# Kernel optimization log

Measured on AMD Instinct MI355X. Metric: run time of the kernel, lower is better.

The kernel has to match this reference:

```python
import jax, jax.numpy as jnp
import numpy as np
from jax import lax

STRIDE = 2
PADDING = 2
KSIZE = 5


def _maxpool3d(y, k):
    # valid max pool with kernel=stride=k over the 3 spatial dims of NCDHW
    return lax.reduce_window(
        y, -jnp.inf, lax.max,
        window_dimensions=(1, 1, k, k, k),
        window_strides=(1, 1, k, k, k),
        padding='VALID')


def setup_inputs() -> dict:
    key = jax.random.key(0)
    k1, k2, k3 = jax.random.split(key, 3)
    x = jax.random.normal(k1, (16, 32, 16, 32, 32), dtype=jnp.float32)
    # torch ConvTranspose3d weight layout: (in_ch, out_ch, kD, kH, kW)
    weight = jax.random.normal(k2, (32, 64, KSIZE, KSIZE, KSIZE), dtype=jnp.float32) * 0.05
    bias = jax.random.normal(k3, (64,), dtype=jnp.float32) * 0.05
    return {"x": x, "weight": weight, "bias": bias}


def reference(x, weight, bias):
    # Fused ConvTranspose3d + sum over output channels.
    # sum_c convT(x, W)[:, c] == convT(x, W.sum(out_ch)) + bias.sum(), so we
    # pre-reduce the weight over the out-channel axis (axis=1) -- same math,
    # and it never materializes the (N, out_ch, D', H', W') intermediate,
    # exactly like the fused CUDA kernel.
    w_sum = weight.sum(axis=1)  # (in_ch, kD, kH, kW)
    # transposed conv == conv with lhs_dilation=stride, pad k-1-p, flipped kernel
    wk = w_sum[None, :, ::-1, ::-1, ::-1]  # (1, in_ch, kD, kH, kW), OIDHW
    pad = KSIZE - 1 - PADDING
    y = lax.conv_general_dilated(
        x, wk,
        window_strides=(1, 1, 1),
        padding=[(pad, pad)] * 3,
        lhs_dilation=(STRIDE, STRIDE, STRIDE),
        dimension_numbers=('NCDHW', 'OIDHW', 'NCDHW'))  # (N,1,31,63,63)
    y = y + bias.sum()
    # MaxPool3d(kernel=2) then MaxPool3d(kernel=3) on the single-channel map
    y = _maxpool3d(y, 2)  # (N,1,15,31,31)
    y = _maxpool3d(y, 3)  # (N,1,5,10,10)
    return y
```

## Files before the change

### kernel.cpp

```cpp
#include <hip/hip_runtime.h>


typedef short v8s __attribute__((ext_vector_type(8)));
typedef float v4f __attribute__((ext_vector_type(4)));
typedef unsigned short ushort_t;

#define CHSTR 16384
#define NSTRIDE (32*CHSTR)
#define Y_N 108000
#define Y_TOT (16*Y_N)
#define XSTR 24

#define PLANE_US 36992u
#define ROW_US 1088u
#define XTN16 591872u
#define BT_BYTE_OFF 18939904u
#define WSF_BYTE_OFF 18967552u
#define NEED_MFMA (18967552u + 4097u*4u)

static __device__ __forceinline__ ushort_t f2bf(float f) {
  unsigned u = __builtin_bit_cast(unsigned, f);
  unsigned r = (u + 0x7FFFu + ((u >> 16) & 1u)) >> 16;
  return (ushort_t)r;
}

__global__ __launch_bounds__(576) void transpose_x(const float* __restrict__ x,
                                                   const float* __restrict__ wt,
                                                   const float* __restrict__ bias,
                                                   ushort_t* __restrict__ xT,
                                                   ushort_t* __restrict__ Btab,
                                                   float* __restrict__ wsf) {
  __shared__ __align__(16) float lb[32 * 264];
  int b = blockIdx.x, t = threadIdx.x;

  if (b >= 256) {
    if (t < 256) {
      int abc = b - 256;
      int a = abc / 9, bb = (abc / 3) % 3, c = abc % 3;
      int half = t & 3;
      int l = t >> 2;
      int tt = l & 15, g = l >> 4;
      float v0 = 0.f, v1 = 0.f;
      if (tt < 8) {
        int td = tt & 1, th = (tt >> 1) & 1, tw = tt >> 2;
        int kd = td + 2 * a, kh = th + 2 * bb, kw = tw + 2 * c;
        if (kd < 5 && kh < 5 && kw < 5) {
          int off = kd * 25 + kh * 5 + kw;
          const float* wp0 = wt + (size_t)(8 * g + 2 * half) * 64 * 125 + off;
          const float* wp1 = wp0 + 64 * 125;
          float s0 = 0.f, s1 = 0.f;
#pragma unroll
          for (int oc = 0; oc < 64; ++oc) { s0 += wp0[oc * 125]; s1 += wp1[oc * 125]; }
          v0 = s0; v1 = s1;
        }
      }
      ((unsigned*)Btab)[(abc * 64 + l) * 4 + half] =
          (unsigned)f2bf(v0) | ((unsigned)f2bf(v1) << 16);
      if (abc == 0 && t == 0) {
        float bs = 0.f;
        for (int o = 0; o < 64; ++o) bs += bias[o];
        wsf[4096] = bs;
      }
    }
    return;
  }

  int tn = 2 * (b & 7) + ((b >> 3) & 1);
  int q  = b >> 4;
  ushort_t* plane = xT + (size_t)(tn * 16 + q) * PLANE_US;
  const float* xb = x + (size_t)tn * NSTRIDE + q * 1024;

  for (int cc = 0; cc < 4; ++cc) {
    for (int j = 0; j < 4; ++j) {
      int s2 = t + 576 * j;
      if (s2 < 2048) {
        int wq = s2 & 7, h8 = (s2 >> 3) & 7, ic = s2 >> 6;
        int h = 8 * cc - 1 + h8;
        if (h >= 0) {
          float4 v = *(const float4*)&xb[(size_t)ic * CHSTR + h * 32 + wq * 4];
          float* L = lb + ic * 264 + h8 * 33 + wq * 4;
          L[0] = v.x; L[1] = v.y; L[2] = v.z; L[3] = v.w;
        }
      }
    }
    __syncthreads();
    for (int j = 0; j < 2; ++j) {
      int s = t + 576 * j;
      if (s < 1088) {
        int icq = s & 3, qq = s >> 2;
        int wslot = qq % 34, r8 = qq / 34;
        int row = 8 * cc + r8;
        ushort_t o[8];
#pragma unroll
        for (int jj = 0; jj < 8; ++jj) o[jj] = 0;
        if (wslot >= 1 && wslot <= 32 && row > 0) {
          int w2 = wslot - 1;
#pragma unroll
          for (int jj = 0; jj < 8; ++jj)
            o[jj] = f2bf(lb[(8 * icq + jj) * 264 + r8 * 33 + w2]);
        }
        uint4 pk;
        pk.x = (unsigned)o[0] | ((unsigned)o[1] << 16);
        pk.y = (unsigned)o[2] | ((unsigned)o[3] << 16);
        pk.z = (unsigned)o[4] | ((unsigned)o[5] << 16);
        pk.w = (unsigned)o[6] | ((unsigned)o[7] << 16);
        *(uint4*)&plane[(size_t)row * ROW_US + wslot * 32 + icq * 8] = pk;
      }
    }
    __syncthreads();
  }
}

__global__ __launch_bounds__(576, 7) void conv_mfma6(const ushort_t* __restrict__ xT,
                                                     const ushort_t* __restrict__ Btab,
                                                     const float* __restrict__ wsf,
                                                     float* __restrict__ out) {
  __shared__ __align__(16) char smem[35328];
  ushort_t* As0 = (ushort_t*)smem;
  ushort_t* As1 = (ushort_t*)(smem + 17408);
  float* ytile  = (float*)smem;
  float* red    = (float*)(smem + 34816);

  int blk = blockIdx.x;
  int xcd = blk & 7;
  int j = blk >> 3;
  int n = 2 * xcd + (j >= 25 ? 1 : 0);
  int cell = (j >= 25) ? j - 25 : j;
  int OD = cell / 5, OH2 = cell % 5;

  int t = threadIdx.x;
  int wv = t >> 6, l = t & 63;
  int mdl = wv / 3, mhp = wv % 3;
  int tt = l & 15, g = l >> 4;

  const ushort_t* xn = xT + (size_t)n * XTN16;
  int rowoff = 6 * OH2 * (int)ROW_US;

  if (OD == 0) {
    for (int jj = 0; jj < 2; ++jj) {
      int s = t + 576 * jj;
      if (s < 1088) *(uint4*)&As0[s * 8] = make_uint4(0, 0, 0, 0);
    }
  } else {
    const ushort_t* slab = xn + (size_t)(3 * OD - 1) * PLANE_US + rowoff;
    uint4 v0 = *(const uint4*)(slab + (size_t)t * 8);
    uint4 v1;
    if (t < 512) v1 = *(const uint4*)(slab + (size_t)(t + 576) * 8);
    *(uint4*)&As0[t * 8] = v0;
    if (t < 512) *(uint4*)&As0[(t + 576) * 8] = v1;
  }
  __syncthreads();

  v4f acc[2][2];
#pragma unroll
  for (int m2 = 0; m2 < 2; ++m2)
#pragma unroll
    for (int wh = 0; wh < 2; ++wh) acc[m2][wh] = (v4f){0.f, 0.f, 0.f, 0.f};

  int lane_base = (2 * mhp) * ROW_US + tt * 32 + g * 8;

  for (int p = 0; p < 5; ++p) {
    uint4 v0, v1;
    if (p < 4) {
      const ushort_t* slab = xn + (size_t)(3 * OD + p) * PLANE_US + rowoff;
      v0 = *(const uint4*)(slab + (size_t)t * 8);
      if (t < 512) v1 = *(const uint4*)(slab + (size_t)(t + 576) * 8);
    }

    int a = mdl + 2 - p;
    if (0 <= a && a <= 2) {
      const ushort_t* Ab = (p & 1) ? As1 : As0;
      const ushort_t* Bg = Btab + ((size_t)(a * 9) * 64 + l) * 8;
      __builtin_amdgcn_s_setprio(1);
#pragma unroll
      for (int c = 0; c < 3; ++c) {
        v8s bv0 = *(const v8s*)(Bg + (0 * 3 + c) * 512);
        v8s bv1 = *(const v8s*)(Bg + (1 * 3 + c) * 512);
        v8s bv2 = *(const v8s*)(Bg + (2 * 3 + c) * 512);
#pragma unroll
        for (int wh = 0; wh < 2; ++wh) {
          const ushort_t* ap = Ab + lane_base + (2 - c + 16 * wh) * 32;
          v8s a0 = *(const v8s*)(ap);
          v8s a1 = *(const v8s*)(ap + 1 * ROW_US);
          v8s a2 = *(const v8s*)(ap + 2 * ROW_US);
          v8s a3 = *(const v8s*)(ap + 3 * ROW_US);
          acc[0][wh] = __builtin_amdgcn_mfma_f32_16x16x32_bf16(a0, bv2, acc[0][wh], 0, 0, 0);
          acc[0][wh] = __builtin_amdgcn_mfma_f32_16x16x32_bf16(a1, bv1, acc[0][wh], 0, 0, 0);
          acc[0][wh] = __builtin_amdgcn_mfma_f32_16x16x32_bf16(a2, bv0, acc[0][wh], 0, 0, 0);
          acc[1][wh] = __builtin_amdgcn_mfma_f32_16x16x32_bf16(a1, bv2, acc[1][wh], 0, 0, 0);
          acc[1][wh] = __builtin_amdgcn_mfma_f32_16x16x32_bf16(a2, bv1, acc[1][wh], 0, 0, 0);
          acc[1][wh] = __builtin_amdgcn_mfma_f32_16x16x32_bf16(a3, bv0, acc[1][wh], 0, 0, 0);
        }
      }
      __builtin_amdgcn_s_setprio(0);
    }

    if (p < 4) {
      ushort_t* dst = (p & 1) ? As0 : As1;
      *(uint4*)&dst[t * 8] = v0;
      if (t < 512) *(uint4*)&dst[(t + 576) * 8] = v1;
      __syncthreads();
    }
  }

  __syncthreads();
  if (tt < 8) {
    int td = tt & 1, th = (tt >> 1) & 1, tw = tt >> 2;
    int odl = 2 * mdl + td;
#pragma unroll
    for (int m2 = 0; m2 < 2; ++m2) {
      int ohl = 2 * (2 * mhp + m2) + th;
      float* yrow = &ytile[(odl * 12 + ohl) * 64];
#pragma unroll
      for (int wh = 0; wh < 2; ++wh)
#pragma unroll
        for (int i = 0; i < 4; ++i)
          yrow[2 * (16 * wh + 4 * g + i) + tw] = acc[m2][wh][i];
    }
  }
  __syncthreads();

  if (t < 120) {
    int OW = t % 10, p_oh = (t / 10) & 1, odl = t / 20;
    float m = -3.4e38f;
    for (int oh = 0; oh < 6; ++oh)
#pragma unroll
      for (int jj = 0; jj < 6; ++jj)
        m = fmaxf(m, ytile[(odl * 12 + 6 * p_oh + oh) * 64 + 6 * OW + jj]);
    red[t] = m;
  }
  __syncthreads();
  if (t < 20) {
    int OW = t % 10, p_oh = t / 10;
    float m = red[p_oh * 10 + OW];
#pragma unroll
    for (int odl = 1; odl < 6; ++odl) m = fmaxf(m, red[odl * 20 + p_oh * 10 + OW]);
    out[((n * 5 + OD) * 10 + (2 * OH2 + p_oh)) * 10 + OW] = m + wsf[4096];
  }
}

__global__ __launch_bounds__(128) void prep2(const float* __restrict__ w,
                                             const float* __restrict__ bias,
                                             float* __restrict__ ws, int woff) {
  int i = blockIdx.x, t = threadIdx.x;
  if (t < 125) {
    const float* wp = w + (size_t)i * 64 * 125 + t;
    float v = 0.f;
#pragma unroll
    for (int o = 0; o < 64; ++o) v += wp[o * 125];
    ws[woff + i * 128 + t] = v;
  }
  if (i == 0 && t == 126) {
    float b = 0.f;
    for (int o = 0; o < 64; ++o) b += bias[o];
    ws[woff + 4096] = b;
  }
}

__global__ __launch_bounds__(256, 4) void conv_stage1(const float* __restrict__ x,
                                                      const float* __restrict__ ws,
                                                      float* part, int woff) {
  __shared__ __align__(16) float xs[170 * XSTR];
  int blk = blockIdx.x;
  int s0 = blk % 320;
  int wq = s0 & 1, hq = (s0 >> 1) & 1, dc = (s0 >> 2) % 5, n = s0 / 20;
  int t = threadIdx.x;
  int mw = t % 15, lmh = t / 15;
  int id_base = 3 * dc - 1, ih_base = 15 * hq - 1;
  int iwb = wq ? 12 : -4;
  int cb = mw + (wq ? 2 : 3);
  const float* xn = x + (size_t)n * NSTRIDE;
  const float* wsw = ws + woff;
  float acc[3][2][2][2] = {{{{0.f}}}};
  for (int phs = 0; phs < 16; ++phs) {
    for (int s = t; s < 1700; s += 256) {
      int c2 = s % 10, row = s / 10;
      int bh = row % 17, q = row / 17;
      int ad = q % 5, lic = q / 5;
      int id = id_base + ad, ih = ih_base + bh, iw = iwb + 2 * c2;
      float2 v = make_float2(0.f, 0.f);
      if ((id | ih | iw) >= 0)
        v = *(const float2*)&xn[(size_t)(phs * 2 + lic) * CHSTR + (id * 32 + ih) * 32 + iw];
      *(float2*)&xs[row * XSTR + 2 * c2] = v;
    }
    __syncthreads();
    if (t < 225) {
#pragma unroll
      for (int lic = 0; lic < 2; ++lic) {
        const float* wc = wsw + (size_t)(phs * 2 + lic) * 128;
        const float* xc = &xs[(lic * 85 + lmh) * XSTR + cb];
        float xv[5][3][3];
#pragma unroll
        for (int a = 0; a < 5; ++a)
#pragma unroll
          for (int b = 0; b < 3; ++b) {
            const float* xr = xc + (a * 17 + b) * XSTR;
            xv[a][b][0] = xr[0]; xv[a][b][1] = xr[1]; xv[a][b][2] = xr[2];
          }
#pragma unroll
        for (int kd = 0; kd < 5; ++kd) {
          constexpr int DT[5] = {0, 1, 0, 1, 0};
          constexpr int AOFF[5] = {2, 2, 1, 1, 0};
          const int dt = DT[kd], aoff = AOFF[kd];
          float wvv[25];
#pragma unroll
          for (int jj = 0; jj < 25; ++jj) wvv[jj] = wc[kd * 25 + jj];
#pragma unroll
          for (int kh = 0; kh < 5; ++kh) {
            constexpr int HT[5] = {0, 1, 0, 1, 0};
            constexpr int BOFF[5] = {2, 2, 1, 1, 0};
            const int ht = HT[kh], boff = BOFF[kh];
#pragma unroll
            for (int m = 0; m < 3; ++m) {
              const float x0 = xv[m + aoff][boff][0];
              const float x1 = xv[m + aoff][boff][1];
              const float x2 = xv[m + aoff][boff][2];
              acc[m][dt][ht][0] += x0 * wvv[kh * 5 + 4];
              acc[m][dt][ht][0] += x1 * wvv[kh * 5 + 2];
              acc[m][dt][ht][0] += x2 * wvv[kh * 5 + 0];
              acc[m][dt][ht][1] += x1 * wvv[kh * 5 + 3];
              acc[m][dt][ht][1] += x2 * wvv[kh * 5 + 1];
            }
          }
        }
      }
    }
    __syncthreads();
  }
  if (t < 225) {
    float* pb = part + (size_t)n * Y_N;
#pragma unroll
    for (int m = 0; m < 3; ++m)
#pragma unroll
      for (int dt = 0; dt < 2; ++dt)
#pragma unroll
        for (int ht = 0; ht < 2; ++ht) {
          int od_g = 6 * dc + 2 * m + dt;
          int oh_g = 30 * hq + 2 * lmh + ht;
          int ow_g = 30 * wq + 2 * mw;
          *(float2*)&pb[(od_g * 60 + oh_g) * 60 + ow_g] =
              make_float2(acc[m][dt][ht][0], acc[m][dt][ht][1]);
        }
  }
}

__global__ __launch_bounds__(256) void pool_stage2(const float* __restrict__ part,
                                                   const float* __restrict__ ws,
                                                   float* __restrict__ out, int woff) {
  __shared__ __align__(16) float buf[2160];
  __shared__ float red[240];
  int blk = blockIdx.x;
  int hc = blk % 10, dc = (blk / 10) % 5, n = blk / 50;
  int t = threadIdx.x;
  const float* pb = part + (size_t)n * Y_N;
  for (int s = t; s < 540; s += 256) {
    int row = s / 15, c4 = s % 15;
    int od = row / 6, oh = row % 6;
    size_t idx = (size_t)((6 * dc + od) * 60 + (6 * hc + oh)) * 60 + 4 * c4;
    *(float4*)&buf[row * 60 + 4 * c4] = *(const float4*)&pb[idx];
  }
  __syncthreads();
  if (t < 240) {
    int wc = t / 24, sub = t % 24;
    float m = -3.4e38f;
#pragma unroll
    for (int k = 0; k < 9; ++k) {
      int e = sub + 24 * k;
      int od = e / 36, r = e % 36;
      int oh = r / 6, ow0 = r % 6;
      m = fmaxf(m, buf[(od * 6 + oh) * 60 + 6 * wc + ow0]);
    }
    red[t] = m;
  }
  __syncthreads();
  if (t < 10) {
    float mm = -3.4e38f;
#pragma unroll
    for (int s2 = 0; s2 < 24; ++s2) mm = fmaxf(mm, red[t * 24 + s2]);
    out[((n * 5 + dc) * 10 + hc) * 10 + t] = mm + ws[woff + 4096];
  }
}

extern "C" void kernel_launch(void* const* d_in, const int* in_sizes, int n_in,
                              void* d_out, int out_size, void* d_ws, size_t ws_size,
                              hipStream_t stream) {
  const float* x    = (const float*)d_in[0];
  const float* w    = (const float*)d_in[1];
  const float* bias = (const float*)d_in[2];
  float* outp = (float*)d_out;

  if (ws_size >= (size_t)NEED_MFMA) {
    ushort_t* xT = (ushort_t*)d_ws;
    ushort_t* Bt = (ushort_t*)((char*)d_ws + BT_BYTE_OFF);
    float* wsf   = (float*)((char*)d_ws + WSF_BYTE_OFF);
    transpose_x<<<256 + 27, 576, 0, stream>>>(x, w, bias, xT, Bt, wsf);
    conv_mfma6<<<400, 576, 0, stream>>>(xT, Bt, wsf, outp);
    return;
  }

  float* ws = (float*)d_ws;
  const size_t need1 = ((size_t)1 * Y_TOT + 4097) * 4;
  if (ws_size >= need1) {
    int woff = Y_TOT;
    prep2<<<32, 128, 0, stream>>>(w, bias, ws, woff);
    conv_stage1<<<320, 256, 0, stream>>>(x, ws, ws, woff);
    pool_stage2<<<800, 256, 0, stream>>>(ws, ws, outp, woff);
  }
}
```

Baseline: 32.09 us.

## Split conv blocks along width into halves to double grid size

The MFMA conv kernel now gives each block half of the output width, so the grid doubles from 400 to 800 blocks. The shared slab per block shrinks to a compacted row layout, and each wave keeps two accumulators instead of four. The goal is more blocks and less LDS per block for better occupancy and load balance across CUs. In exchange, neighbouring halves reload overlapping input halo columns and B-table loads, and the weight fetches are amortized over less work.

Measured after the change: 34.81 us. 8.5% more time.

```diff
diff --git a/kernel.cpp b/kernel.cpp
--- a/kernel.cpp
+++ b/kernel.cpp
@@ -17,6 +17,8 @@
 #define BT_BYTE_OFF 18939904u
 #define WSF_BYTE_OFF 18967552u
 #define NEED_MFMA (18967552u + 4097u*4u)
+
+#define SLAB_ROW 576
 
 static __device__ __forceinline__ ushort_t f2bf(float f) {
   unsigned u = __builtin_bit_cast(unsigned, f);
@@ -111,22 +113,24 @@
   }
 }
 
-__global__ __launch_bounds__(576, 7) void conv_mfma6(const ushort_t* __restrict__ xT,
+__global__ __launch_bounds__(576, 7) void conv_mfma8(const ushort_t* __restrict__ xT,
                                                      const ushort_t* __restrict__ Btab,
                                                      const float* __restrict__ wsf,
                                                      float* __restrict__ out) {
-  __shared__ __align__(16) char smem[35328];
+  __shared__ __align__(16) char smem[18672];
   ushort_t* As0 = (ushort_t*)smem;
-  ushort_t* As1 = (ushort_t*)(smem + 17408);
+  ushort_t* As1 = (ushort_t*)(smem + 9216);
   float* ytile  = (float*)smem;
-  float* red    = (float*)(smem + 34816);
+  float* red    = (float*)(smem + 18432);
 
   int blk = blockIdx.x;
   int xcd = blk & 7;
   int j = blk >> 3;
-  int n = 2 * xcd + (j >= 25 ? 1 : 0);
-  int cell = (j >= 25) ? j - 25 : j;
-  int OD = cell / 5, OH2 = cell % 5;
+  int n = 2 * xcd + (j >= 50 ? 1 : 0);
+  int c50 = (j >= 50) ? j - 50 : j;
+  int OD = c50 / 10;
+  int r10 = c50 % 10;
+  int OH2 = r10 >> 1, h = r10 & 1;
 
   int t = threadIdx.x;
   int wv = t >> 6, l = t & 63;
@@ -134,38 +138,29 @@
   int tt = l & 15, g = l >> 4;
 
   const ushort_t* xn = xT + (size_t)n * XTN16;
-  int rowoff = 6 * OH2 * (int)ROW_US;
+  const ushort_t* slabb = xn + (size_t)(6 * OH2) * ROW_US + 15 * h * 32;
+  int r8 = t / 72, inner = t % 72;
+  int colrel = inner >> 2, icq = inner & 3;
+  size_t soff = (size_t)r8 * ROW_US + colrel * 32 + icq * 8;
+  int doff = r8 * SLAB_ROW + colrel * 32 + icq * 8;
 
   if (OD == 0) {
-    for (int jj = 0; jj < 2; ++jj) {
-      int s = t + 576 * jj;
-      if (s < 1088) *(uint4*)&As0[s * 8] = make_uint4(0, 0, 0, 0);
-    }
+    *(uint4*)&As0[t * 16 / 2] = make_uint4(0, 0, 0, 0);
   } else {
-    const ushort_t* slab = xn + (size_t)(3 * OD - 1) * PLANE_US + rowoff;
-    uint4 v0 = *(const uint4*)(slab + (size_t)t * 8);
-    uint4 v1;
-    if (t < 512) v1 = *(const uint4*)(slab + (size_t)(t + 576) * 8);
-    *(uint4*)&As0[t * 8] = v0;
-    if (t < 512) *(uint4*)&As0[(t + 576) * 8] = v1;
-  }
-  __syncthreads();
-
-  v4f acc[2][2];
-#pragma unroll
-  for (int m2 = 0; m2 < 2; ++m2)
-#pragma unroll
-    for (int wh = 0; wh < 2; ++wh) acc[m2][wh] = (v4f){0.f, 0.f, 0.f, 0.f};
-
-  int lane_base = (2 * mhp) * ROW_US + tt * 32 + g * 8;
+    uint4 v0 = *(const uint4*)(slabb + (size_t)(3 * OD - 1) * PLANE_US + soff);
+    *(uint4*)&As0[doff] = v0;
+  }
+  __syncthreads();
+
+  v4f acc[2];
+  acc[0] = (v4f){0.f, 0.f, 0.f, 0.f};
+  acc[1] = (v4f){0.f, 0.f, 0.f, 0.f};
+
+  int lane_base = (2 * mhp) * SLAB_ROW + tt * 32 + g * 8;
 
   for (int p = 0; p < 5; ++p) {
-    uint4 v0, v1;
-    if (p < 4) {
-      const ushort_t* slab = xn + (size_t)(3 * OD + p) * PLANE_US + rowoff;
-      v0 = *(const uint4*)(slab + (size_t)t * 8);
-      if (t < 512) v1 = *(const uint4*)(slab + (size_t)(t + 576) * 8);
-    }
+    uint4 v0;
+    if (p < 4) v0 = *(const uint4*)(slabb + (size_t)(3 * OD + p) * PLANE_US + soff);
 
     int a = mdl + 2 - p;
     if (0 <= a && a <= 2) {
@@ -177,28 +172,24 @@
         v8s bv0 = *(const v8s*)(Bg + (0 * 3 + c) * 512);
         v8s bv1 = *(const v8s*)(Bg + (1 * 3 + c) * 512);
         v8s bv2 = *(const v8s*)(Bg + (2 * 3 + c) * 512);
-#pragma unroll
-        for (int wh = 0; wh < 2; ++wh) {
-          const ushort_t* ap = Ab + lane_base + (2 - c + 16 * wh) * 32;
-          v8s a0 = *(const v8s*)(ap);
-          v8s a1 = *(const v8s*)(ap + 1 * ROW_US);
-          v8s a2 = *(const v8s*)(ap + 2 * ROW_US);
-          v8s a3 = *(const v8s*)(ap + 3 * ROW_US);
-          acc[0][wh] = __builtin_amdgcn_mfma_f32_16x16x32_bf16(a0, bv2, acc[0][wh], 0, 0, 0);
-          acc[0][wh] = __builtin_amdgcn_mfma_f32_16x16x32_bf16(a1, bv1, acc[0][wh], 0, 0, 0);
-          acc[0][wh] = __builtin_amdgcn_mfma_f32_16x16x32_bf16(a2, bv0, acc[0][wh], 0, 0, 0);
-          acc[1][wh] = __builtin_amdgcn_mfma_f32_16x16x32_bf16(a1, bv2, acc[1][wh], 0, 0, 0);
-          acc[1][wh] = __builtin_amdgcn_mfma_f32_16x16x32_bf16(a2, bv1, acc[1][wh], 0, 0, 0);
-          acc[1][wh] = __builtin_amdgcn_mfma_f32_16x16x32_bf16(a3, bv0, acc[1][wh], 0, 0, 0);
-        }
+        const ushort_t* ap = Ab + lane_base + (2 - c) * 32;
+        v8s a0 = *(const v8s*)(ap);
+        v8s a1 = *(const v8s*)(ap + 1 * SLAB_ROW);
+        v8s a2 = *(const v8s*)(ap + 2 * SLAB_ROW);
+        v8s a3 = *(const v8s*)(ap + 3 * SLAB_ROW);
+        acc[0] = __builtin_amdgcn_mfma_f32_16x16x32_bf16(a0, bv2, acc[0], 0, 0, 0);
+        acc[0] = __builtin_amdgcn_mfma_f32_16x16x32_bf16(a1, bv1, acc[0], 0, 0, 0);
+        acc[0] = __builtin_amdgcn_mfma_f32_16x16x32_bf16(a2, bv0, acc[0], 0, 0, 0);
+        acc[1] = __builtin_amdgcn_mfma_f32_16x16x32_bf16(a1, bv2, acc[1], 0, 0, 0);
+        acc[1] = __builtin_amdgcn_mfma_f32_16x16x32_bf16(a2, bv1, acc[1], 0, 0, 0);
+        acc[1] = __builtin_amdgcn_mfma_f32_16x16x32_bf16(a3, bv0, acc[1], 0, 0, 0);
       }
       __builtin_amdgcn_s_setprio(0);
     }
 
     if (p < 4) {
       ushort_t* dst = (p & 1) ? As0 : As1;
-      *(uint4*)&dst[t * 8] = v0;
-      if (t < 512) *(uint4*)&dst[(t + 576) * 8] = v1;
+      *(uint4*)&dst[doff] = v0;
       __syncthreads();
     }
   }
@@ -210,32 +201,32 @@
 #pragma unroll
     for (int m2 = 0; m2 < 2; ++m2) {
       int ohl = 2 * (2 * mhp + m2) + th;
-      float* yrow = &ytile[(odl * 12 + ohl) * 64];
-#pragma unroll
-      for (int wh = 0; wh < 2; ++wh)
-#pragma unroll
-        for (int i = 0; i < 4; ++i)
-          yrow[2 * (16 * wh + 4 * g + i) + tw] = acc[m2][wh][i];
-    }
-  }
-  __syncthreads();
-
-  if (t < 120) {
-    int OW = t % 10, p_oh = (t / 10) & 1, odl = t / 20;
+      float* yrow = &ytile[(odl * 12 + ohl) * 32];
+#pragma unroll
+      for (int i = 0; i < 4; ++i) {
+        int mwD = 4 * g + i;
+        if (mwD < 15) yrow[2 * mwD + tw] = acc[m2][i];
+      }
+    }
+  }
+  __syncthreads();
+
+  if (t < 60) {
+    int OWloc = t % 5, p_oh = (t / 5) & 1, odl = t / 10;
     float m = -3.4e38f;
     for (int oh = 0; oh < 6; ++oh)
 #pragma unroll
       for (int jj = 0; jj < 6; ++jj)
-        m = fmaxf(m, ytile[(odl * 12 + 6 * p_oh + oh) * 64 + 6 * OW + jj]);
+        m = fmaxf(m, ytile[(odl * 12 + 6 * p_oh + oh) * 32 + 6 * OWloc + jj]);
     red[t] = m;
   }
   __syncthreads();
-  if (t < 20) {
-    int OW = t % 10, p_oh = t / 10;
-    float m = red[p_oh * 10 + OW];
-#pragma unroll
-    for (int odl = 1; odl < 6; ++odl) m = fmaxf(m, red[odl * 20 + p_oh * 10 + OW]);
-    out[((n * 5 + OD) * 10 + (2 * OH2 + p_oh)) * 10 + OW] = m + wsf[4096];
+  if (t < 10) {
+    int p_oh = t / 5, OWloc = t % 5;
+    float m = red[p_oh * 5 + OWloc];
+#pragma unroll
+    for (int odl = 1; odl < 6; ++odl) m = fmaxf(m, red[odl * 10 + p_oh * 5 + OWloc]);
+    out[((n * 5 + OD) * 10 + (2 * OH2 + p_oh)) * 10 + 5 * h + OWloc] = m + wsf[4096];
   }
 }
 
@@ -394,7 +385,7 @@
     ushort_t* Bt = (ushort_t*)((char*)d_ws + BT_BYTE_OFF);
     float* wsf   = (float*)((char*)d_ws + WSF_BYTE_OFF);
     transpose_x<<<256 + 27, 576, 0, stream>>>(x, w, bias, xT, Bt, wsf);
-    conv_mfma6<<<400, 576, 0, stream>>>(xT, Bt, wsf, outp);
+    conv_mfma8<<<800, 576, 0, stream>>>(xT, Bt, wsf, outp);
     return;
   }
 
```
